# Kernel optimization log

Hardware: AMD Instinct MI355X
Metric: run time of the kernel (lower is better)

## Reference

```python
import jax, jax.numpy as jnp
import numpy as np

EMB = 1024
HEADS = 16
HD = EMB // HEADS

def setup_inputs() -> dict:
    key = jax.random.key(0)
    ks = jax.random.split(key, 9)
    s = 1.0 / np.sqrt(EMB)
    x = jax.random.normal(ks[0], (4, 2048, EMB), dtype=jnp.float32)
    Wq = jax.random.uniform(ks[1], (EMB, EMB), jnp.float32, -s, s)
    bq = jax.random.uniform(ks[2], (EMB,), jnp.float32, -s, s)
    Wk = jax.random.uniform(ks[3], (EMB, EMB), jnp.float32, -s, s)
    bk = jax.random.uniform(ks[4], (EMB,), jnp.float32, -s, s)
    Wv = jax.random.uniform(ks[5], (EMB, EMB), jnp.float32, -s, s)
    bv = jax.random.uniform(ks[6], (EMB,), jnp.float32, -s, s)
    Wo = jax.random.uniform(ks[7], (EMB, EMB), jnp.float32, -s, s)
    bo = jax.random.uniform(ks[8], (EMB,), jnp.float32, -s, s)
    return {"x": x, "Wq": Wq, "bq": bq, "Wk": Wk, "bk": bk, "Wv": Wv, "bv": bv, "Wo": Wo, "bo": bo}

def reference(x, Wq, bq, Wk, bk, Wv, bv, Wo, bo):
    B, T, C = x.shape
    # projections (torch Linear: y = x @ W^T + b)
    q = (x @ Wq.T + bq).reshape(B, T, HEADS, HD).transpose(0, 2, 1, 3)  # [B,H,T,hd]
    k = (x @ Wk.T + bk).reshape(B, T, HEADS, HD).transpose(0, 2, 1, 3)
    v = (x @ Wv.T + bv).reshape(B, T, HEADS, HD).transpose(0, 2, 1, 3)
    scores = jnp.einsum('bhqd,bhkd->bhqk', q, k) / jnp.sqrt(jnp.float32(HD))
    weights = jax.nn.softmax(scores, axis=-1)
    attn = jnp.einsum('bhqk,bhkd->bhqd', weights, v)
    out = attn.transpose(0, 2, 1, 3).reshape(B, T, C)
    return out @ Wo.T + bo
```

## Files before the change

kernel.cpp:

```cpp
#include <hip/hip_runtime.h>

#define TSEQ  2048
#define BATCH 4
#define NHEAD 16
#define EMB   1024

typedef __attribute__((ext_vector_type(8))) __bf16 bf16x8;
typedef __attribute__((ext_vector_type(4))) __bf16 bf16x4;
typedef __attribute__((ext_vector_type(4))) float  floatx4;
typedef __attribute__((ext_vector_type(2))) unsigned int uint32x2;
typedef __attribute__((ext_vector_type(4))) unsigned int uint32x4;

__device__ __forceinline__ void gload_lds16(const __bf16* g, __bf16* lds_uniform_base) {
  __builtin_amdgcn_global_load_lds(
      (__attribute__((address_space(1))) void*)(g),
      (__attribute__((address_space(3))) void*)(lds_uniform_base),
      16, 0, 0);
}

__global__ __launch_bounds__(256) void cvt_f32_bf16(
    const float* __restrict__ src, __bf16* __restrict__ dst)
{
  const int gid = (blockIdx.x * 256 + threadIdx.x) * 4;
  const float4 v = *(const float4*)(src + gid);
  dst[gid + 0] = (__bf16)v.x;
  dst[gid + 1] = (__bf16)v.y;
  dst[gid + 2] = (__bf16)v.z;
  dst[gid + 3] = (__bf16)v.w;
}

__global__ __launch_bounds__(256) void cvt_w4(
    const float* __restrict__ s0, const float* __restrict__ s1,
    const float* __restrict__ s2, const float* __restrict__ s3,
    __bf16* __restrict__ d0, __bf16* __restrict__ d1,
    __bf16* __restrict__ d2, __bf16* __restrict__ d3)
{
  const int z = blockIdx.z;
  const float* src = (z == 0) ? s0 : (z == 1) ? s1 : (z == 2) ? s2 : s3;
  __bf16*      dst = (z == 0) ? d0 : (z == 1) ? d1 : (z == 2) ? d2 : d3;
  const int gid = (blockIdx.x * 256 + threadIdx.x) * 4;
  const float4 v = *(const float4*)(src + gid);
  dst[gid + 0] = (__bf16)v.x;
  dst[gid + 1] = (__bf16)v.y;
  dst[gid + 2] = (__bf16)v.z;
  dst[gid + 3] = (__bf16)v.w;
}

__global__ __launch_bounds__(256) void gemm_bt_bias(
    const __bf16* __restrict__ A,
    const __bf16* __restrict__ W0, const __bf16* __restrict__ W1, const __bf16* __restrict__ W2,
    const float* __restrict__ B0, const float* __restrict__ B1, const float* __restrict__ B2,
    __bf16* __restrict__ C0, __bf16* __restrict__ C1, __bf16* __restrict__ C2)
{
  const int z = blockIdx.z;
  const __bf16* W  = (z == 0) ? W0 : ((z == 1) ? W1 : W2);
  const float*  Bb = (z == 0) ? B0 : ((z == 1) ? B1 : B2);
  __bf16*       C  = (z == 0) ? C0 : ((z == 1) ? C1 : C2);
  const float  scl = (z == 0) ? 0.125f * 1.44269504088896340736f : 1.0f;

  const int tid  = threadIdx.x;
  const int lane = tid & 63;
  const int wid  = tid >> 6;
  const int l16  = lane & 15;
  const int quad = lane >> 4;
  const int wm   = wid & 1;
  const int wn   = wid >> 1;
  const int lin = blockIdx.x + blockIdx.y * 8;
  const int swz = (lin & 7) * 64 + (lin >> 3);
  const int m0  = (swz >> 3) * 128;
  const int n0  = (swz & 7) * 128;

  __shared__ alignas(16) __bf16 As[128 * 32];
  __shared__ alignas(16) __bf16 Bs[128 * 32];

  floatx4 acc[4][4];
#pragma unroll
  for (int i = 0; i < 4; i++)
#pragma unroll
    for (int j = 0; j < 4; j++) acc[i][j] = (floatx4){0.f, 0.f, 0.f, 0.f};

  const int srow = tid >> 2;
  const int sseg = tid & 3;

  for (int k0 = 0; k0 < 1024; k0 += 32) {
    __syncthreads();
#pragma unroll
    for (int is = 0; is < 2; is++) {
      const int row = is * 64 + srow;
      gload_lds16(A + (size_t)(m0 + row) * 1024 + k0 + sseg * 8,
                  &As[(is * 256 + wid * 64) * 8]);
      gload_lds16(W + (size_t)(n0 + row) * 1024 + k0 + sseg * 8,
                  &Bs[(is * 256 + wid * 64) * 8]);
    }
    __syncthreads();

    bf16x8 af[4], bfr[4];
#pragma unroll
    for (int i = 0; i < 4; i++) {
      af[i]  = *(const bf16x8*)(&As[(wm * 64 + i * 16 + l16) * 32 + quad * 8]);
      bfr[i] = *(const bf16x8*)(&Bs[(wn * 64 + i * 16 + l16) * 32 + quad * 8]);
    }
#pragma unroll
    for (int i = 0; i < 4; i++)
#pragma unroll
      for (int j = 0; j < 4; j++)
        acc[i][j] = __builtin_amdgcn_mfma_f32_16x16x32_bf16(af[i], bfr[j], acc[i][j], 0, 0, 0);
  }

  float bv[4];
#pragma unroll
  for (int j = 0; j < 4; j++) bv[j] = Bb[n0 + wn * 64 + j * 16 + l16];

#pragma unroll
  for (int i = 0; i < 4; i++) {
    const size_t mrow = (size_t)m0 + wm * 64 + i * 16 + quad * 4;
#pragma unroll
    for (int j = 0; j < 4; j++) {
      const int col = n0 + wn * 64 + j * 16 + l16;
#pragma unroll
      for (int r = 0; r < 4; r++)
        C[(mrow + r) * 1024 + col] = (__bf16)((acc[i][j][r] + bv[j]) * scl);
    }
  }
}

__global__ __launch_bounds__(256) void gemm_bt_bias_f32(
    const __bf16* __restrict__ A, const __bf16* __restrict__ W,
    const float* __restrict__ Bb, float* __restrict__ C)
{
  const int tid  = threadIdx.x;
  const int lane = tid & 63;
  const int wid  = tid >> 6;
  const int l16  = lane & 15;
  const int quad = lane >> 4;
  const int wm   = wid & 1;
  const int wn   = wid >> 1;
  const int lin = blockIdx.x + blockIdx.y * 8;
  const int swz = (lin & 7) * 64 + (lin >> 3);
  const int m0  = (swz >> 3) * 128;
  const int n0  = (swz & 7) * 128;

  __shared__ alignas(16) __bf16 As[128 * 32];
  __shared__ alignas(16) __bf16 Bs[128 * 32];

  floatx4 acc[4][4];
#pragma unroll
  for (int i = 0; i < 4; i++)
#pragma unroll
    for (int j = 0; j < 4; j++) acc[i][j] = (floatx4){0.f, 0.f, 0.f, 0.f};

  const int srow = tid >> 2;
  const int sseg = tid & 3;

  for (int k0 = 0; k0 < 1024; k0 += 32) {
    __syncthreads();
#pragma unroll
    for (int is = 0; is < 2; is++) {
      const int row = is * 64 + srow;
      gload_lds16(A + (size_t)(m0 + row) * 1024 + k0 + sseg * 8,
                  &As[(is * 256 + wid * 64) * 8]);
      gload_lds16(W + (size_t)(n0 + row) * 1024 + k0 + sseg * 8,
                  &Bs[(is * 256 + wid * 64) * 8]);
    }
    __syncthreads();

    bf16x8 af[4], bfr[4];
#pragma unroll
    for (int i = 0; i < 4; i++) {
      af[i]  = *(const bf16x8*)(&As[(wm * 64 + i * 16 + l16) * 32 + quad * 8]);
      bfr[i] = *(const bf16x8*)(&Bs[(wn * 64 + i * 16 + l16) * 32 + quad * 8]);
    }
#pragma unroll
    for (int i = 0; i < 4; i++)
#pragma unroll
      for (int j = 0; j < 4; j++)
        acc[i][j] = __builtin_amdgcn_mfma_f32_16x16x32_bf16(af[i], bfr[j], acc[i][j], 0, 0, 0);
  }

  float bv[4];
#pragma unroll
  for (int j = 0; j < 4; j++) bv[j] = Bb[n0 + wn * 64 + j * 16 + l16];

#pragma unroll
  for (int i = 0; i < 4; i++) {
    const size_t mrow = (size_t)m0 + wm * 64 + i * 16 + quad * 4;
#pragma unroll
    for (int j = 0; j < 4; j++) {
      const int col = n0 + wn * 64 + j * 16 + l16;
#pragma unroll
      for (int r = 0; r < 4; r++)
        C[(mrow + r) * 1024 + col] = acc[i][j][r] + bv[j];
    }
  }
}

__global__ __launch_bounds__(256) void v_transpose(
    const __bf16* __restrict__ V, __bf16* __restrict__ VT)
{
  const int t0 = blockIdx.x * 64;
  const int bh = blockIdx.y;
  const int b  = bh >> 4;
  const int h  = bh & 15;
  const int tid = threadIdx.x;

  __shared__ alignas(16) __bf16 Ls[64 * 72];

  const int row = tid >> 2, seg = tid & 3;
  const __bf16* src = V + ((size_t)(b * TSEQ + t0 + row)) * EMB + h * 64;
  *(bf16x8*)(&Ls[row * 72 + seg * 8])       = *(const bf16x8*)(src + seg * 8);
  *(bf16x8*)(&Ls[row * 72 + (seg + 4) * 8]) = *(const bf16x8*)(src + (seg + 4) * 8);
  __syncthreads();

  const int od = tid >> 2, oseg = tid & 3;
  bf16x8 o0, o1;
#pragma unroll
  for (int j = 0; j < 8; j++) o0[j] = Ls[(oseg * 16 + j) * 72 + od];
#pragma unroll
  for (int j = 0; j < 8; j++) o1[j] = Ls[(oseg * 16 + 8 + j) * 72 + od];
  __bf16* dst = VT + ((size_t)bh * 64 + od) * TSEQ + t0 + oseg * 16;
  *(bf16x8*)(dst)     = o0;
  *(bf16x8*)(dst + 8) = o1;
}

#define KVB 64
#define NT  (TSEQ / KVB)

#define FA_STAGE(BUF, TILE)                                                               \
  if ((TILE) < NT) {                                                                      \
    _Pragma("unroll")                                                                     \
    for (int c = 0; c < 2; c++) {                                                         \
      gload_lds16(kstage + (size_t)((TILE) * KVB + c * 8) * EMB,                          \
                  &Ks[BUF][(wid * 16 + c * 8) * 64]);                                     \
      gload_lds16(vstage + (size_t)(c * 8) * TSEQ + (TILE) * KVB,                         \
                  &VTs[BUF][(wid * 16 + c * 8) * 64]);                                    \
    }                                                                                     \
  }

#define FA_STEP(BUF, KT)                                                                  \
  {                                                                                       \
    FA_STAGE((BUF) ^ 1, (KT) + 1);                                                        \
    __builtin_amdgcn_s_setprio(1);                                                        \
    bf16x8 pfrag[4][2];                                                                   \
    _Pragma("unroll")                                                                     \
    for (int ks = 0; ks < 2; ks++) {                                                      \
      const bf16x8 ka0 = *(const bf16x8*)(&Ks[BUF][ks * 2048 + aoff0]);                   \
      const bf16x8 ka1 = *(const bf16x8*)(&Ks[BUF][ks * 2048 + aoff1]);                   \
      const bf16x8 kb0 = *(const bf16x8*)(&Ks[BUF][ks * 2048 + 1024 + aoff0]);            \
      const bf16x8 kb1 = *(const bf16x8*)(&Ks[BUF][ks * 2048 + 1024 + aoff1]);            \
      _Pragma("unroll")                                                                   \
      for (int g = 0; g < 4; g++) {                                                       \
        floatx4 ta = (floatx4){0.f, 0.f, 0.f, 0.f};                                       \
        floatx4 tb = (floatx4){0.f, 0.f, 0.f, 0.f};                                       \
        ta = __builtin_amdgcn_mfma_f32_16x16x32_bf16(ka0, qf[g][0], ta, 0, 0, 0);         \
        ta = __builtin_amdgcn_mfma_f32_16x16x32_bf16(ka1, qf[g][1], ta, 0, 0, 0);         \
        tb = __builtin_amdgcn_mfma_f32_16x16x32_bf16(kb0, qf[g][0], tb, 0, 0, 0);         \
        tb = __builtin_amdgcn_mfma_f32_16x16x32_bf16(kb1, qf[g][1], tb, 0, 0, 0);         \
        bf16x4 pa, pb;                                                                    \
        _Pragma("unroll")                                                                 \
        for (int r = 0; r < 4; r++) pa[r] = (__bf16)__builtin_amdgcn_exp2f(ta[r]);        \
        _Pragma("unroll")                                                                 \
        for (int r = 0; r < 4; r++) pb[r] = (__bf16)__builtin_amdgcn_exp2f(tb[r]);        \
        const uint32x2 A2 = __builtin_bit_cast(uint32x2, pa);                             \
        const uint32x2 B2 = __builtin_bit_cast(uint32x2, pb);                             \
        const uint32x2 r0 = __builtin_amdgcn_permlane32_swap(A2.x, B2.x, false, false);   \
        const uint32x2 r1 = __builtin_amdgcn_permlane32_swap(A2.y, B2.y, false, false);   \
        const uint32x2 s0 = __builtin_amdgcn_permlane16_swap(r0.x, r0.y, false, false);   \
        const uint32x2 s1 = __builtin_amdgcn_permlane16_swap(r1.x, r1.y, false, false);   \
        const uint32x4 fw = (uint32x4){s0.x, s1.x, s0.y, s1.y};                           \
        pfrag[g][ks] = __builtin_bit_cast(bf16x8, fw);                                    \
      }                                                                                   \
    }                                                                                     \
    _Pragma("unroll")                                                                     \
    for (int g = 0; g < 4; g++) {                                                         \
      lacc[g] = __builtin_amdgcn_mfma_f32_16x16x32_bf16(ones, pfrag[g][0], lacc[g], 0, 0, 0); \
      lacc[g] = __builtin_amdgcn_mfma_f32_16x16x32_bf16(ones, pfrag[g][1], lacc[g], 0, 0, 0); \
    }                                                                                     \
    _Pragma("unroll")                                                                     \
    for (int dg = 0; dg < 4; dg++) {                                                      \
      _Pragma("unroll")                                                                   \
      for (int ks = 0; ks < 2; ks++) {                                                    \
        const bf16x8 vf = *(const bf16x8*)(&VTs[BUF][dg * 1024 + (ks ? aoff1 : aoff0)]);  \
        _Pragma("unroll")                                                                 \
        for (int g = 0; g < 4; g++)                                                       \
          Oacc[g][dg] = __builtin_amdgcn_mfma_f32_16x16x32_bf16(vf, pfrag[g][ks], Oacc[g][dg], 0, 0, 0); \
      }                                                                                   \
    }                                                                                     \
    __builtin_amdgcn_s_setprio(0);                                                        \
    __syncthreads();                                                                      \
  }

__global__ __launch_bounds__(256, 2) void flash_attn(
    const __bf16* __restrict__ Q, const __bf16* __restrict__ K,
    const __bf16* __restrict__ VT, __bf16* __restrict__ O)
{
  const int lin = blockIdx.x + blockIdx.y * 8;
  const int swz = (lin & 7) * 64 + (lin >> 3);
  const int qt  = swz & 7;
  const int bh  = swz >> 3;
  const int b    = bh >> 4;
  const int h    = bh & 15;
  const int tid  = threadIdx.x;
  const int wid  = tid >> 6;
  const int lane = tid & 63;
  const int l16  = lane & 15;
  const int quad = lane >> 4;

  __shared__ alignas(16) __bf16 Ks[2][KVB * 64];
  __shared__ alignas(16) __bf16 VTs[2][64 * 64];

  const size_t base = ((size_t)b * TSEQ) * EMB + (size_t)h * 64;
  const __bf16* qptr  = Q + base;
  const __bf16* kptr  = K + base;
  const __bf16* vtptr = VT + (size_t)bh * 64 * TSEQ;
  __bf16*       optr  = O + base;

  const int qb = qt * 256 + wid * 64;

  bf16x8 qf[4][2];
#pragma unroll
  for (int g = 0; g < 4; g++)
#pragma unroll
    for (int hf = 0; hf < 2; hf++)
      qf[g][hf] = *(const bf16x8*)(qptr + (size_t)(qb + g * 16 + l16) * EMB + hf * 32 + quad * 8);

  floatx4 Oacc[4][4];
#pragma unroll
  for (int g = 0; g < 4; g++)
#pragma unroll
    for (int dg = 0; dg < 4; dg++) Oacc[g][dg] = (floatx4){0.f, 0.f, 0.f, 0.f};
  floatx4 lacc[4];
#pragma unroll
  for (int g = 0; g < 4; g++) lacc[g] = (floatx4){0.f, 0.f, 0.f, 0.f};

  const uint32x4 onesw = (uint32x4){0x3F803F80u, 0x3F803F80u, 0x3F803F80u, 0x3F803F80u};
  const bf16x8 ones = __builtin_bit_cast(bf16x8, onesw);

  const int lrow = lane >> 3;
  const int xsg  = (lane & 7) ^ lrow;
  const __bf16* kstage = kptr  + (size_t)(wid * 16 + lrow) * EMB  + xsg * 8;
  const __bf16* vstage = vtptr + (size_t)(wid * 16 + lrow) * TSEQ + xsg * 8;

  const int h7    = l16 & 7;
  const int x0    = quad ^ h7;
  const int aoff0 = l16 * 64 + x0 * 8;
  const int aoff1 = l16 * 64 + (x0 ^ 4) * 8;

  FA_STAGE(0, 0);
  __syncthreads();

#pragma unroll 1
  for (int kt = 0; kt < NT; kt += 2) {
    FA_STEP(0, kt);
    FA_STEP(1, kt + 1);
  }

#pragma unroll
  for (int g = 0; g < 4; g++) {
    const float inv = 1.0f / lacc[g][0];
#pragma unroll
    for (int dg = 0; dg < 4; dg++) {
      bf16x4 ov;
#pragma unroll
      for (int r = 0; r < 4; r++) ov[r] = (__bf16)(Oacc[g][dg][r] * inv);
      *(bf16x4*)(optr + (size_t)(qb + g * 16 + l16) * EMB + dg * 16 + quad * 4) = ov;
    }
  }
}

extern "C" void kernel_launch(void* const* d_in, const int* in_sizes, int n_in,
                              void* d_out, int out_size, void* d_ws, size_t ws_size,
                              hipStream_t stream) {
  const float* x  = (const float*)d_in[0];
  const float* Wq = (const float*)d_in[1];
  const float* bq = (const float*)d_in[2];
  const float* Wk = (const float*)d_in[3];
  const float* bk = (const float*)d_in[4];
  const float* Wv = (const float*)d_in[5];
  const float* bv = (const float*)d_in[6];
  const float* Wo = (const float*)d_in[7];
  const float* bo = (const float*)d_in[8];
  float* out = (float*)d_out;

  const size_t NELEM = (size_t)BATCH * TSEQ * EMB;
  const size_t WELEM = (size_t)EMB * EMB;

  __bf16* q_b  = (__bf16*)d_out;
  __bf16* k_b  = q_b + NELEM;
  __bf16* x_b  = (__bf16*)d_ws;
  __bf16* v_b  = x_b + NELEM;
  __bf16* wq_b = v_b + NELEM;
  __bf16* wk_b = wq_b + WELEM;
  __bf16* wv_b = wk_b + WELEM;
  __bf16* wo_b = wv_b + WELEM;

  dim3 blk(256, 1, 1);

  cvt_f32_bf16<<<(int)(NELEM / 1024), blk, 0, stream>>>(x, x_b);
  cvt_w4<<<dim3((int)(WELEM / 1024), 1, 4), blk, 0, stream>>>(
      Wq, Wk, Wv, Wo, wq_b, wk_b, wv_b, wo_b);

  gemm_bt_bias<<<dim3(8, 64, 3), blk, 0, stream>>>(
      x_b, wq_b, wk_b, wv_b, bq, bk, bv, q_b, k_b, v_b);

  v_transpose<<<dim3(TSEQ / 64, BATCH * NHEAD), blk, 0, stream>>>(v_b, x_b);

  flash_attn<<<dim3(TSEQ / 256, BATCH * NHEAD), blk, 0, stream>>>(
      q_b, k_b, x_b, v_b);

  gemm_bt_bias_f32<<<dim3(8, 64, 1), blk, 0, stream>>>(v_b, wo_b, bo, out);
}
```

Baseline: 265.3 us.

## Software-pipeline flash attention: overlap next tile's QK/exp with previous tile's PV

Restructures the flash-attention inner loop so that the QK^T scores and exp/pack for tile k+1 are computed while the PV MFMAs for tile k run, carrying P fragments across iterations in pfragP. A prologue computes the first tile's P and an epilogue does the final PV. The stage load now comes after a barrier in mid-step. The aim is to hide the exp/permlane latency behind matrix ops, at the cost of more live registers and an extra barrier per step.

```diff
diff --git a/kernel.cpp b/kernel.cpp
--- a/kernel.cpp
+++ b/kernel.cpp
@@ -225,6 +225,8 @@
 #define KVB 64
 #define NT  (TSEQ / KVB)
 
+#define FA_ZERO (floatx4){0.f, 0.f, 0.f, 0.f}
+
 #define FA_STAGE(BUF, TILE)                                                               \
   if ((TILE) < NT) {                                                                      \
     _Pragma("unroll")                                                                     \
@@ -236,56 +238,71 @@
     }                                                                                     \
   }
 
+#define SM_PACK(TA, TB, DST)                                                              \
+  {                                                                                       \
+    bf16x4 pa_, pb_;                                                                      \
+    _Pragma("unroll")                                                                     \
+    for (int r = 0; r < 4; r++) pa_[r] = (__bf16)__builtin_amdgcn_exp2f((TA)[r]);         \
+    _Pragma("unroll")                                                                     \
+    for (int r = 0; r < 4; r++) pb_[r] = (__bf16)__builtin_amdgcn_exp2f((TB)[r]);         \
+    const uint32x2 A2_ = __builtin_bit_cast(uint32x2, pa_);                               \
+    const uint32x2 B2_ = __builtin_bit_cast(uint32x2, pb_);                               \
+    const uint32x2 r0_ = __builtin_amdgcn_permlane32_swap(A2_.x, B2_.x, false, false);    \
+    const uint32x2 r1_ = __builtin_amdgcn_permlane32_swap(A2_.y, B2_.y, false, false);    \
+    const uint32x2 s0_ = __builtin_amdgcn_permlane16_swap(r0_.x, r0_.y, false, false);    \
+    const uint32x2 s1_ = __builtin_amdgcn_permlane16_swap(r1_.x, r1_.y, false, false);    \
+    const uint32x4 fw_ = (uint32x4){s0_.x, s1_.x, s0_.y, s1_.y};                          \
+    DST = __builtin_bit_cast(bf16x8, fw_);                                                \
+  }
+
+#define QK_BLOCK(BUF, KS, TA, TB)                                                         \
+  {                                                                                       \
+    const bf16x8 ka0 = *(const bf16x8*)(&Ks[BUF][(KS) * 2048 + aoff0]);                   \
+    const bf16x8 ka1 = *(const bf16x8*)(&Ks[BUF][(KS) * 2048 + aoff1]);                   \
+    const bf16x8 kb0 = *(const bf16x8*)(&Ks[BUF][(KS) * 2048 + 1024 + aoff0]);            \
+    const bf16x8 kb1 = *(const bf16x8*)(&Ks[BUF][(KS) * 2048 + 1024 + aoff1]);            \
+    _Pragma("unroll")                                                                     \
+    for (int g = 0; g < 4; g++) {                                                         \
+      TA[g] = FA_ZERO;                                                                    \
+      TA[g] = __builtin_amdgcn_mfma_f32_16x16x32_bf16(ka0, qf[g][0], TA[g], 0, 0, 0);     \
+      TA[g] = __builtin_amdgcn_mfma_f32_16x16x32_bf16(ka1, qf[g][1], TA[g], 0, 0, 0);     \
+      TB[g] = FA_ZERO;                                                                    \
+      TB[g] = __builtin_amdgcn_mfma_f32_16x16x32_bf16(kb0, qf[g][0], TB[g], 0, 0, 0);     \
+      TB[g] = __builtin_amdgcn_mfma_f32_16x16x32_bf16(kb1, qf[g][1], TB[g], 0, 0, 0);     \
+    }                                                                                     \
+  }
+
 #define FA_STEP(BUF, KT)                                                                  \
   {                                                                                       \
+    __builtin_amdgcn_s_setprio(1);                                                        \
+    bf16x8 vf[4][2];                                                                      \
+    _Pragma("unroll")                                                                     \
+    for (int dg = 0; dg < 4; dg++) {                                                      \
+      vf[dg][0] = *(const bf16x8*)(&VTs[(BUF) ^ 1][dg * 1024 + aoff0]);                   \
+      vf[dg][1] = *(const bf16x8*)(&VTs[(BUF) ^ 1][dg * 1024 + aoff1]);                   \
+    }                                                                                     \
+    floatx4 ta[4], tb[4];                                                                 \
+    QK_BLOCK(BUF, 0, ta, tb)                                                              \
+    _Pragma("unroll")                                                                     \
+    for (int g = 0; g < 4; g++) {                                                         \
+      bf16x8 nf;                                                                          \
+      SM_PACK(ta[g], tb[g], nf)                                                           \
+      _Pragma("unroll")                                                                   \
+      for (int dg = 0; dg < 4; dg++)                                                      \
+        Oacc[g][dg] = __builtin_amdgcn_mfma_f32_16x16x32_bf16(vf[dg][0], pfragP[g][0], Oacc[g][dg], 0, 0, 0); \
+      lacc[g] = __builtin_amdgcn_mfma_f32_16x16x32_bf16(ones, pfragP[g][0], lacc[g], 0, 0, 0); \
+      _Pragma("unroll")                                                                   \
+      for (int dg = 0; dg < 4; dg++)                                                      \
+        Oacc[g][dg] = __builtin_amdgcn_mfma_f32_16x16x32_bf16(vf[dg][1], pfragP[g][1], Oacc[g][dg], 0, 0, 0); \
+      lacc[g] = __builtin_amdgcn_mfma_f32_16x16x32_bf16(ones, pfragP[g][1], lacc[g], 0, 0, 0); \
+      pfragP[g][0] = nf;                                                                  \
+    }                                                                                     \
+    QK_BLOCK(BUF, 1, ta, tb)                                                              \
+    __builtin_amdgcn_s_setprio(0);                                                        \
+    __syncthreads();                                                                      \
     FA_STAGE((BUF) ^ 1, (KT) + 1);                                                        \
-    __builtin_amdgcn_s_setprio(1);                                                        \
-    bf16x8 pfrag[4][2];                                                                   \
-    _Pragma("unroll")                                                                     \
-    for (int ks = 0; ks < 2; ks++) {                                                      \
-      const bf16x8 ka0 = *(const bf16x8*)(&Ks[BUF][ks * 2048 + aoff0]);                   \
-      const bf16x8 ka1 = *(const bf16x8*)(&Ks[BUF][ks * 2048 + aoff1]);                   \
-      const bf16x8 kb0 = *(const bf16x8*)(&Ks[BUF][ks * 2048 + 1024 + aoff0]);            \
-      const bf16x8 kb1 = *(const bf16x8*)(&Ks[BUF][ks * 2048 + 1024 + aoff1]);            \
-      _Pragma("unroll")                                                                   \
-      for (int g = 0; g < 4; g++) {                                                       \
-        floatx4 ta = (floatx4){0.f, 0.f, 0.f, 0.f};                                       \
-        floatx4 tb = (floatx4){0.f, 0.f, 0.f, 0.f};                                       \
-        ta = __builtin_amdgcn_mfma_f32_16x16x32_bf16(ka0, qf[g][0], ta, 0, 0, 0);         \
-        ta = __builtin_amdgcn_mfma_f32_16x16x32_bf16(ka1, qf[g][1], ta, 0, 0, 0);         \
-        tb = __builtin_amdgcn_mfma_f32_16x16x32_bf16(kb0, qf[g][0], tb, 0, 0, 0);         \
-        tb = __builtin_amdgcn_mfma_f32_16x16x32_bf16(kb1, qf[g][1], tb, 0, 0, 0);         \
-        bf16x4 pa, pb;                                                                    \
-        _Pragma("unroll")                                                                 \
-        for (int r = 0; r < 4; r++) pa[r] = (__bf16)__builtin_amdgcn_exp2f(ta[r]);        \
-        _Pragma("unroll")                                                                 \
-        for (int r = 0; r < 4; r++) pb[r] = (__bf16)__builtin_amdgcn_exp2f(tb[r]);        \
-        const uint32x2 A2 = __builtin_bit_cast(uint32x2, pa);                             \
-        const uint32x2 B2 = __builtin_bit_cast(uint32x2, pb);                             \
-        const uint32x2 r0 = __builtin_amdgcn_permlane32_swap(A2.x, B2.x, false, false);   \
-        const uint32x2 r1 = __builtin_amdgcn_permlane32_swap(A2.y, B2.y, false, false);   \
-        const uint32x2 s0 = __builtin_amdgcn_permlane16_swap(r0.x, r0.y, false, false);   \
-        const uint32x2 s1 = __builtin_amdgcn_permlane16_swap(r1.x, r1.y, false, false);   \
-        const uint32x4 fw = (uint32x4){s0.x, s1.x, s0.y, s1.y};                           \
-        pfrag[g][ks] = __builtin_bit_cast(bf16x8, fw);                                    \
-      }                                                                                   \
-    }                                                                                     \
-    _Pragma("unroll")                                                                     \
-    for (int g = 0; g < 4; g++) {                                                         \
-      lacc[g] = __builtin_amdgcn_mfma_f32_16x16x32_bf16(ones, pfrag[g][0], lacc[g], 0, 0, 0); \
-      lacc[g] = __builtin_amdgcn_mfma_f32_16x16x32_bf16(ones, pfrag[g][1], lacc[g], 0, 0, 0); \
-    }                                                                                     \
-    _Pragma("unroll")                                                                     \
-    for (int dg = 0; dg < 4; dg++) {                                                      \
-      _Pragma("unroll")                                                                   \
-      for (int ks = 0; ks < 2; ks++) {                                                    \
-        const bf16x8 vf = *(const bf16x8*)(&VTs[BUF][dg * 1024 + (ks ? aoff1 : aoff0)]);  \
-        _Pragma("unroll")                                                                 \
-        for (int g = 0; g < 4; g++)                                                       \
-          Oacc[g][dg] = __builtin_amdgcn_mfma_f32_16x16x32_bf16(vf, pfrag[g][ks], Oacc[g][dg], 0, 0, 0); \
-      }                                                                                   \
-    }                                                                                     \
-    __builtin_amdgcn_s_setprio(0);                                                        \
+    _Pragma("unroll")                                                                     \
+    for (int g = 0; g < 4; g++) { SM_PACK(ta[g], tb[g], pfragP[g][1]) }                   \
     __syncthreads();                                                                      \
   }
 
@@ -327,10 +344,10 @@
 #pragma unroll
   for (int g = 0; g < 4; g++)
 #pragma unroll
-    for (int dg = 0; dg < 4; dg++) Oacc[g][dg] = (floatx4){0.f, 0.f, 0.f, 0.f};
+    for (int dg = 0; dg < 4; dg++) Oacc[g][dg] = FA_ZERO;
   floatx4 lacc[4];
 #pragma unroll
-  for (int g = 0; g < 4; g++) lacc[g] = (floatx4){0.f, 0.f, 0.f, 0.f};
+  for (int g = 0; g < 4; g++) lacc[g] = FA_ZERO;
 
   const uint32x4 onesw = (uint32x4){0x3F803F80u, 0x3F803F80u, 0x3F803F80u, 0x3F803F80u};
   const bf16x8 ones = __builtin_bit_cast(bf16x8, onesw);
@@ -345,13 +362,40 @@
   const int aoff0 = l16 * 64 + x0 * 8;
   const int aoff1 = l16 * 64 + (x0 ^ 4) * 8;
 
+  bf16x8 pfragP[4][2];
+
   FA_STAGE(0, 0);
   __syncthreads();
+  FA_STAGE(1, 1);
+  {
+    floatx4 ta[4], tb[4];
+    QK_BLOCK(0, 0, ta, tb)
+#pragma unroll
+    for (int g = 0; g < 4; g++) { SM_PACK(ta[g], tb[g], pfragP[g][0]) }
+    QK_BLOCK(0, 1, ta, tb)
+#pragma unroll
+    for (int g = 0; g < 4; g++) { SM_PACK(ta[g], tb[g], pfragP[g][1]) }
+  }
+  __syncthreads();
 
 #pragma unroll 1
-  for (int kt = 0; kt < NT; kt += 2) {
-    FA_STEP(0, kt);
-    FA_STEP(1, kt + 1);
+  for (int kt = 1; kt < NT - 1; kt += 2) {
+    FA_STEP(1, kt);
+    FA_STEP(0, kt + 1);
+  }
+  FA_STEP(1, NT - 1);
+
+#pragma unroll
+  for (int g = 0; g < 4; g++) {
+#pragma unroll
+    for (int dg = 0; dg < 4; dg++) {
+      const bf16x8 v0 = *(const bf16x8*)(&VTs[1][dg * 1024 + aoff0]);
+      const bf16x8 v1 = *(const bf16x8*)(&VTs[1][dg * 1024 + aoff1]);
+      Oacc[g][dg] = __builtin_amdgcn_mfma_f32_16x16x32_bf16(v0, pfragP[g][0], Oacc[g][dg], 0, 0, 0);
+      Oacc[g][dg] = __builtin_amdgcn_mfma_f32_16x16x32_bf16(v1, pfragP[g][1], Oacc[g][dg], 0, 0, 0);
+    }
+    lacc[g] = __builtin_amdgcn_mfma_f32_16x16x32_bf16(ones, pfragP[g][0], lacc[g], 0, 0, 0);
+    lacc[g] = __builtin_amdgcn_mfma_f32_16x16x32_bf16(ones, pfragP[g][1], lacc[g], 0, 0, 0);
   }
 
 #pragma unroll
```

Result: no change. 261.1 us (-1.6%).
